# Kernel tuning notes

Hardware: AMD Instinct MI355X
Metric: run time of the kernel (lower is better)

Reference implementation:

```python
import jax, jax.numpy as jnp
import numpy as np

B, N, C = 4, 4096, 768
H = 8
HD = C // H  # head_dim = 96
SCALE = HD ** -0.5
EPS = 1e-12  # torch F.normalize eps


def setup_inputs() -> dict:
    key = jax.random.key(0)
    ks = jax.random.split(key, 6)
    s = C ** -0.5
    return {
        "context_x": jax.random.normal(ks[0], (B, N, C), dtype=jnp.float32),
        "depth_x": jax.random.normal(ks[1], (B, N, C), dtype=jnp.float32),
        "Wq": jax.random.normal(ks[2], (C, C), dtype=jnp.float32) * s,
        "Wkv": jax.random.normal(ks[3], (C, 2 * C), dtype=jnp.float32) * s,
        "Wproj": jax.random.normal(ks[4], (C, C), dtype=jnp.float32) * s,
        "bproj": jax.random.normal(ks[5], (C,), dtype=jnp.float32) * 0.01,
    }


def _l2norm(x):
    # matches torch.nn.functional.normalize(x, dim=-1)
    n = jnp.sqrt(jnp.sum(x * x, axis=-1, keepdims=True))
    return x / jnp.maximum(n, EPS)


def reference(context_x, depth_x, Wq, Wkv, Wproj, bproj):
    b, n, c = context_x.shape
    # projections
    q = (context_x @ Wq).reshape(b, n, H, HD).transpose(0, 2, 3, 1)  # [B,H,hd,N]
    kv = (depth_x @ Wkv).reshape(b, n, 2, H, HD)
    k = kv[:, :, 0].transpose(0, 2, 3, 1)  # [B,H,hd,N]
    v = kv[:, :, 1].transpose(0, 2, 3, 1)  # [B,H,hd,N]
    # cosine-normalize over the token axis (last dim after transpose)
    q = _l2norm(q)
    k = _l2norm(k)
    # channel-attention (cross-covariance): attn is [B,H,hd,hd]
    attn = jnp.einsum("bhdn,bhen->bhde", q, k) * SCALE
    attn = jax.nn.softmax(attn, axis=-1)
    x = jnp.einsum("bhde,bhen->bhdn", attn, v)  # [B,H,hd,N]
    x = x.transpose(0, 3, 1, 2).reshape(b, n, c)  # [B,N,C]
    return x @ Wproj + bproj
```

## Files before the change

kernel.cpp:

```cpp
#include <hip/hip_runtime.h>


using bf16x8 = __attribute__((ext_vector_type(8))) short;
using f32x4  = __attribute__((ext_vector_type(4))) float;

#define SCALE_ 0.10206207261596575f

__device__ __forceinline__ unsigned short f2bf(float f) {
    unsigned int u = __builtin_bit_cast(unsigned int, f);
    u += 0x7FFFu + ((u >> 16) & 1u);
    return (unsigned short)(u >> 16);
}
__device__ __forceinline__ float bf2f(unsigned short h) {
    unsigned int u = ((unsigned int)h) << 16;
    return __builtin_bit_cast(float, u);
}

__device__ __forceinline__ void glds16(const unsigned short* g, unsigned short* l) {
    __builtin_amdgcn_global_load_lds(
        (const __attribute__((address_space(1))) void*)g,
        (__attribute__((address_space(3))) void*)l, 16, 0, 0);
}

__device__ __forceinline__ float ssq8(bf16x8 v) {
    uint4 u = __builtin_bit_cast(uint4, v);
    unsigned a[4] = {u.x, u.y, u.z, u.w};
    float s = 0.f;
    #pragma unroll
    for (int i = 0; i < 4; i++) {
        float lo = __builtin_bit_cast(float, a[i] << 16);
        float hi = __builtin_bit_cast(float, a[i] & 0xFFFF0000u);
        s += lo * lo + hi * hi;
    }
    return s;
}

__global__ void f32_to_bf16_k(const float* __restrict__ in,
                              unsigned short* __restrict__ out)
{
    size_t idx = ((size_t)blockIdx.x * 256 + threadIdx.x) * 8;
    float4 v0 = *(const float4*)&in[idx];
    float4 v1 = *(const float4*)&in[idx + 4];
    unsigned short h[8];
    h[0] = f2bf(v0.x); h[1] = f2bf(v0.y); h[2] = f2bf(v0.z); h[3] = f2bf(v0.w);
    h[4] = f2bf(v1.x); h[5] = f2bf(v1.y); h[6] = f2bf(v1.z); h[7] = f2bf(v1.w);
    *(bf16x8*)&out[idx] = *(bf16x8*)h;
}

__global__ void transpose_to_bf16(const float* __restrict__ W,
                                  unsigned short* __restrict__ Wt,
                                  int K, int N)
{
    __shared__ float tile[32][33];
    int n0 = blockIdx.x * 32, k0 = blockIdx.y * 32;
    int tx = threadIdx.x, ty = threadIdx.y;
    #pragma unroll
    for (int i = 0; i < 32; i += 8)
        tile[ty + i][tx] = W[(size_t)(k0 + ty + i) * N + n0 + tx];
    __syncthreads();
    #pragma unroll
    for (int i = 0; i < 32; i += 8)
        Wt[(size_t)(n0 + ty + i) * K + k0 + tx] = f2bf(tile[tx][ty + i]);
}

template<int MODE>
__global__ __launch_bounds__(256) void gemm_bt(
    const unsigned short* __restrict__ A, const unsigned short* __restrict__ Bt,
    const float* __restrict__ bias, void* __restrict__ out0, void* __restrict__ out1,
    int M, int N, int K)
{
    __shared__ unsigned short As[128 * 32];
    __shared__ unsigned short Bs[128 * 32];

    const int Nt = gridDim.x, Mt = gridDim.y;
    const int lin = blockIdx.y * Nt + blockIdx.x;
    const int xcd = lin & 7, li = lin >> 3;
    const int band = Mt >> 3;
    const int mt = xcd * band + (li % band);
    const int nt = li / band;
    const int bm = mt * 128, bn = nt * 128;

    const int t = threadIdx.x, lane = t & 63, w = t >> 6;
    const int wm = (w >> 1) * 64, wn = (w & 1) * 64;
    const int mf = lane & 15, quad = lane >> 4;

    const int srow = lane & 15, skc = (lane >> 4) * 8;
    const unsigned short* gA = A  + (size_t)(bm + w * 32 + srow) * K + skc;
    const unsigned short* gB = Bt + (size_t)(bn + w * 32 + srow) * K + skc;

    f32x4 acc[4][4] = {};

    for (int k0 = 0; k0 < K; k0 += 32) {
        #pragma unroll
        for (int c = 0; c < 2; c++) {
            glds16(gA + (size_t)(c * 16) * K + k0, &As[(w * 2 + c) * 512]);
            glds16(gB + (size_t)(c * 16) * K + k0, &Bs[(w * 2 + c) * 512]);
        }
        __syncthreads();
        bf16x8 a[4], b[4];
        #pragma unroll
        for (int i = 0; i < 4; i++)
            a[i] = *(const bf16x8*)&As[(((w >> 1) * 4) + i) * 512 + lane * 8];
        #pragma unroll
        for (int j = 0; j < 4; j++)
            b[j] = *(const bf16x8*)&Bs[(((w & 1) * 4) + j) * 512 + lane * 8];
        #pragma unroll
        for (int i = 0; i < 4; i++)
            #pragma unroll
            for (int j = 0; j < 4; j++)
                acc[i][j] = __builtin_amdgcn_mfma_f32_16x16x32_bf16(a[i], b[j], acc[i][j], 0, 0, 0);
        __syncthreads();
    }

    if constexpr (MODE == 2) {
        float* C = (float*)out0;
        #pragma unroll
        for (int i = 0; i < 4; i++) {
            int row0 = bm + wm + i * 16 + quad * 4;
            #pragma unroll
            for (int j = 0; j < 4; j++) {
                int col = bn + wn + j * 16 + mf;
                float bv = bias[col];
                #pragma unroll
                for (int r = 0; r < 4; r++)
                    C[(size_t)(row0 + r) * N + col] = acc[i][j][r] + bv;
            }
        }
    } else {
        unsigned short* Tr = (unsigned short*)out0;
        unsigned short* Vb = (unsigned short*)out1;
        const bool kpart = (MODE == 0) || (bn < 768);
        #pragma unroll
        for (int i = 0; i < 4; i++) {
            int row0 = bm + wm + i * 16 + quad * 4;
            int bb = row0 >> 12, n = row0 & 4095;
            #pragma unroll
            for (int j = 0; j < 4; j++) {
                int c = bn + wn + j * 16 + mf;
                if (kpart) {
                    int h = (c * 683) >> 16;
                    int d = c - h * 96;
                    size_t o = ((size_t)((bb * 8 + h) * 96 + d)) * 4096 + n;
                    ushort4 v4;
                    v4.x = f2bf(acc[i][j][0]); v4.y = f2bf(acc[i][j][1]);
                    v4.z = f2bf(acc[i][j][2]); v4.w = f2bf(acc[i][j][3]);
                    *(ushort4*)&Tr[o] = v4;
                } else {
                    int cv = c - 768;
                    #pragma unroll
                    for (int r = 0; r < 4; r++)
                        Vb[(size_t)(row0 + r) * 768 + cv] = f2bf(acc[i][j][r]);
                }
            }
        }
    }
}

__global__ __launch_bounds__(256) void s_gemm(
    const unsigned short* __restrict__ Qt, const unsigned short* __restrict__ Kt,
    float* __restrict__ Spart, float* __restrict__ ssq)
{
    __shared__ unsigned short Qs[2][12 * 512];
    __shared__ unsigned short Ks[2][12 * 512];
    const int s = blockIdx.x, bh = blockIdx.y;
    const int t = threadIdx.x, lane = t & 63, w = t >> 6;
    const int m0 = (w >> 1) * 48, n0w = (w & 1) * 48;
    const int mf = lane & 15, quad = lane >> 4;
    const int srow = lane & 15, skc = (lane >> 4) * 8;
    const int nwin = s * 512;

    const unsigned short* Qg = Qt + (size_t)bh * 96 * 4096;
    const unsigned short* Kg = Kt + (size_t)bh * 96 * 4096;

    f32x4 acc[3][3] = {};
    float sq[3] = {0.f, 0.f, 0.f}, sk[3] = {0.f, 0.f, 0.f};

    #pragma unroll
    for (int c = 0; c < 3; c++) {
        int bi = w * 3 + c, kc = bi / 6, g = bi % 6;
        size_t go = (size_t)(g * 16 + srow) * 4096 + nwin + kc * 32 + skc;
        glds16(Qg + go, &Qs[0][bi * 512]);
        glds16(Kg + go, &Ks[0][bi * 512]);
    }

    for (int it = 0; it < 8; it++) {
        const int cur = it & 1;
        __syncthreads();
        if (it + 1 < 8) {
            const int nxt = cur ^ 1;
            const int nn = nwin + (it + 1) * 64;
            #pragma unroll
            for (int c = 0; c < 3; c++) {
                int bi = w * 3 + c, kc = bi / 6, g = bi % 6;
                size_t go = (size_t)(g * 16 + srow) * 4096 + nn + kc * 32 + skc;
                glds16(Qg + go, &Qs[nxt][bi * 512]);
                glds16(Kg + go, &Ks[nxt][bi * 512]);
            }
        }
        #pragma unroll
        for (int kk = 0; kk < 2; kk++) {
            bf16x8 a[3], b[3];
            #pragma unroll
            for (int i = 0; i < 3; i++)
                a[i] = *(const bf16x8*)&Qs[cur][(kk * 6 + (w >> 1) * 3 + i) * 512 + lane * 8];
            #pragma unroll
            for (int j = 0; j < 3; j++)
                b[j] = *(const bf16x8*)&Ks[cur][(kk * 6 + (w & 1) * 3 + j) * 512 + lane * 8];
            if ((w & 1) == 0) {
                #pragma unroll
                for (int i = 0; i < 3; i++) sq[i] += ssq8(a[i]);
            }
            if ((w >> 1) == 0) {
                #pragma unroll
                for (int j = 0; j < 3; j++) sk[j] += ssq8(b[j]);
            }
            #pragma unroll
            for (int i = 0; i < 3; i++)
                #pragma unroll
                for (int j = 0; j < 3; j++)
                    acc[i][j] = __builtin_amdgcn_mfma_f32_16x16x32_bf16(a[i], b[j], acc[i][j], 0, 0, 0);
        }
    }

    if ((w & 1) == 0) {
        #pragma unroll
        for (int i = 0; i < 3; i++) {
            float v = sq[i];
            v += __shfl_xor(v, 16, 64);
            v += __shfl_xor(v, 32, 64);
            if (lane < 16) atomicAdd(&ssq[bh * 96 + m0 + i * 16 + lane], v);
        }
    }
    if ((w >> 1) == 0) {
        #pragma unroll
        for (int j = 0; j < 3; j++) {
            float v = sk[j];
            v += __shfl_xor(v, 16, 64);
            v += __shfl_xor(v, 32, 64);
            if (lane < 16) atomicAdd(&ssq[3072 + bh * 96 + n0w + j * 16 + lane], v);
        }
    }

    float* outp = Spart + (size_t)(bh * 8 + s) * 9216;
    #pragma unroll
    for (int i = 0; i < 3; i++)
        #pragma unroll
        for (int j = 0; j < 3; j++) {
            int e  = n0w + j * 16 + mf;
            int d0 = m0 + i * 16 + quad * 4;
            #pragma unroll
            for (int r = 0; r < 4; r++)
                outp[(d0 + r) * 96 + e] = acc[i][j][r];
        }
}

__global__ __launch_bounds__(256) void softmax_k(
    const float* __restrict__ Spart, const float* __restrict__ ssq,
    unsigned short* __restrict__ P)
{
    const int bh = blockIdx.y;
    const int d  = blockIdx.x * 4 + (threadIdx.x >> 6);
    const int lane = threadIdx.x & 63;

    const float sr = SCALE_ / fmaxf(sqrtf(ssq[bh * 96 + d]), 1e-12f);

    const float* Sp = Spart + (size_t)bh * 8 * 9216 + d * 96;
    float sa = 0.f, sb = 0.f;
    #pragma unroll
    for (int ch = 0; ch < 8; ch++) {
        sa += Sp[ch * 9216 + lane];
        if (lane < 32) sb += Sp[ch * 9216 + 64 + lane];
    }
    float ka = 1.0f / fmaxf(sqrtf(ssq[3072 + bh * 96 + lane]), 1e-12f);
    float va = sa * sr * ka;
    float vb = -1e30f;
    if (lane < 32) {
        float kb = 1.0f / fmaxf(sqrtf(ssq[3072 + bh * 96 + 64 + lane]), 1e-12f);
        vb = sb * sr * kb;
    }

    float m = fmaxf(va, vb);
    #pragma unroll
    for (int off = 32; off >= 1; off >>= 1)
        m = fmaxf(m, __shfl_xor(m, off, 64));

    float ea = __expf(va - m);
    float eb = (lane < 32) ? __expf(vb - m) : 0.f;
    float ssum = ea + eb;
    #pragma unroll
    for (int off = 32; off >= 1; off >>= 1)
        ssum += __shfl_xor(ssum, off, 64);

    float inv = 1.0f / ssum;
    unsigned short* Pr = P + (size_t)bh * 9216 + d * 96;
    Pr[lane] = f2bf(ea * inv);
    if (lane < 32) Pr[64 + lane] = f2bf(eb * inv);
}

__global__ __launch_bounds__(256) void pv_gemm(
    const unsigned short* __restrict__ Vb, const unsigned short* __restrict__ P,
    unsigned short* __restrict__ X)
{
    __shared__ unsigned short Ps[96][104];
    int ntile = blockIdx.x, bh = blockIdx.y;
    int b = bh >> 3, h = bh & 7;
    int t = threadIdx.x, lane = t & 63, w = t >> 6;

    const unsigned short* Pg = P + (size_t)bh * 9216;
    #pragma unroll
    for (int i = 0; i < 9; i++) {
        int idx4 = t + 256 * i;
        int row = idx4 / 24, c4 = (idx4 - row * 24) * 4;
        *(ushort4*)&Ps[row][c4] = *(const ushort4*)&Pg[row * 96 + c4];
    }
    __syncthreads();

    const unsigned short* Vbase = Vb + (size_t)b * 4096 * 768 + h * 96;
    int mf = lane & 15, k8 = (lane >> 4) * 8;
    f32x4 acc[2][6] = {};
    #pragma unroll
    for (int k = 0; k < 3; k++) {
        bf16x8 a[2], bb[6];
        #pragma unroll
        for (int i = 0; i < 2; i++) {
            int row = ntile * 128 + w * 32 + i * 16 + mf;
            a[i] = *(const bf16x8*)&Vbase[(size_t)row * 768 + k * 32 + k8];
        }
        #pragma unroll
        for (int j = 0; j < 6; j++)
            bb[j] = *(const bf16x8*)&Ps[j * 16 + mf][k * 32 + k8];
        #pragma unroll
        for (int i = 0; i < 2; i++)
            #pragma unroll
            for (int j = 0; j < 6; j++)
                acc[i][j] = __builtin_amdgcn_mfma_f32_16x16x32_bf16(a[i], bb[j], acc[i][j], 0, 0, 0);
    }
    #pragma unroll
    for (int i = 0; i < 2; i++)
        #pragma unroll
        for (int j = 0; j < 6; j++)
            #pragma unroll
            for (int r = 0; r < 4; r++) {
                int n_tok = ntile * 128 + w * 32 + i * 16 + (lane >> 4) * 4 + r;
                int c = h * 96 + j * 16 + mf;
                X[((size_t)b * 4096 + n_tok) * 768 + c] = f2bf(acc[i][j][r]);
            }
}

extern "C" void kernel_launch(void* const* d_in, const int* in_sizes, int n_in,
                              void* d_out, int out_size, void* d_ws, size_t ws_size,
                              hipStream_t stream)
{
    (void)in_sizes; (void)n_in; (void)out_size; (void)ws_size;
    const float* ctx   = (const float*)d_in[0];
    const float* dep   = (const float*)d_in[1];
    const float* Wq    = (const float*)d_in[2];
    const float* Wkv   = (const float*)d_in[3];
    const float* Wproj = (const float*)d_in[4];
    const float* bproj = (const float*)d_in[5];
    float* out = (float*)d_out;

    char* p = (char*)d_ws;
    auto carve = [&](size_t bytes) {
        char* r = p;
        p += (bytes + 255) & ~(size_t)255;
        return r;
    };
    unsigned short* WqT    = (unsigned short*)carve((size_t)768 * 768 * 2);
    unsigned short* WkvT   = (unsigned short*)carve((size_t)1536 * 768 * 2);
    unsigned short* WprojT = (unsigned short*)carve((size_t)768 * 768 * 2);
    unsigned short* Qt     = (unsigned short*)carve((size_t)32 * 96 * 4096 * 2);
    unsigned short* Kt     = (unsigned short*)carve((size_t)32 * 96 * 4096 * 2);
    unsigned short* Vb     = (unsigned short*)carve((size_t)16384 * 768 * 2);
    unsigned short* Xb     = (unsigned short*)carve((size_t)16384 * 768 * 2);
    float*          ssq    = (float*)carve((size_t)2 * 3072 * 4);
    float*          Spart  = (float*)carve((size_t)32 * 8 * 9216 * 4);
    unsigned short* Pb     = (unsigned short*)carve((size_t)32 * 9216 * 2);
    unsigned short* depB   = (unsigned short*)carve((size_t)16384 * 768 * 2);
    unsigned short* ctxB   = Xb;

    hipMemsetAsync(ssq, 0, 2 * 3072 * 4, stream);

    f32_to_bf16_k<<<6144, 256, 0, stream>>>(ctx, ctxB);
    f32_to_bf16_k<<<6144, 256, 0, stream>>>(dep, depB);

    dim3 tb(32, 8);
    transpose_to_bf16<<<dim3(24, 24), tb, 0, stream>>>(Wq, WqT, 768, 768);
    transpose_to_bf16<<<dim3(48, 24), tb, 0, stream>>>(Wkv, WkvT, 768, 1536);
    transpose_to_bf16<<<dim3(24, 24), tb, 0, stream>>>(Wproj, WprojT, 768, 768);

    gemm_bt<0><<<dim3(6, 128), 256, 0, stream>>>(ctxB, WqT, nullptr, Qt, nullptr, 16384, 768, 768);
    gemm_bt<1><<<dim3(12, 128), 256, 0, stream>>>(depB, WkvT, nullptr, Kt, Vb, 16384, 1536, 768);

    s_gemm<<<dim3(8, 32), 256, 0, stream>>>(Qt, Kt, Spart, ssq);
    softmax_k<<<dim3(24, 32), 256, 0, stream>>>(Spart, ssq, Pb);
    pv_gemm<<<dim3(32, 32), 256, 0, stream>>>(Vb, Pb, Xb);
    gemm_bt<2><<<dim3(6, 128), 256, 0, stream>>>(Xb, WprojT, bproj, out, nullptr, 16384, 768, 768);
}
```

Measured before the change: 237.3 us.

## Rewrite projection GEMMs as 256x256 tiles with double-buffered ping-pong pipeline

Replaces the 128x128, 256-thread, single-buffer GEMM with a 256x256 tile, 512-thread kernel. It double-buffers LDS, splits each 64-wide K step into four MFMA quadrants interleaved with async global-to-LDS loads, and adds explicit vmcnt waits, barriers and setprio to overlap memory with compute. The larger tile raises operand reuse, and the schedule hides load latency. In exchange it uses more LDS and registers (launch bounds 512,2) and gives fewer blocks: 192 or 384 on a 256-CU part, which may hurt occupancy and wave balance.

```diff
diff --git a/kernel.cpp b/kernel.cpp
--- a/kernel.cpp
+++ b/kernel.cpp
@@ -63,14 +63,80 @@
         Wt[(size_t)(n0 + ty + i) * K + k0 + tx] = f2bf(tile[tx][ty + i]);
 }
 
+
+#define BAR __builtin_amdgcn_s_barrier()
+#define VM(n) asm volatile("s_waitcnt vmcnt(" #n ")" ::: "memory")
+
+#define ST_A(buf, tt, h) do { \
+    _Pragma("unroll") \
+    for (int c_ = 0; c_ < 2; c_++) \
+        glds16(gA + (size_t)(((h) * 8 + w) * 16) * K + (size_t)(tt) * 64 + c_ * 32, \
+               &As[buf][(c_ * 16 + (h) * 8 + w) * 512]); \
+} while (0)
+
+#define ST_B(buf, tt, h) do { \
+    _Pragma("unroll") \
+    for (int c_ = 0; c_ < 2; c_++) \
+        glds16(gB + (size_t)(((h) * 8 + w) * 16) * K + (size_t)(tt) * 64 + c_ * 32, \
+               &Bs[buf][(c_ * 16 + (h) * 8 + w) * 512]); \
+} while (0)
+
+#define RD_A(buf, mh) do { \
+    _Pragma("unroll") \
+    for (int i_ = 0; i_ < 4; i_++) \
+    _Pragma("unroll") \
+    for (int kk_ = 0; kk_ < 2; kk_++) \
+        a[i_][kk_] = *(const bf16x8*)&As[buf][(kk_ * 16 + wr * 8 + (mh) * 4 + i_) * 512 + lane * 8]; \
+} while (0)
+
+#define RD_B(buf, nh) do { \
+    _Pragma("unroll") \
+    for (int j_ = 0; j_ < 2; j_++) \
+    _Pragma("unroll") \
+    for (int kk_ = 0; kk_ < 2; kk_++) \
+        b[nh][j_][kk_] = *(const bf16x8*)&Bs[buf][(kk_ * 16 + wc * 4 + (nh) * 2 + j_) * 512 + lane * 8]; \
+} while (0)
+
+#define MM(mh, nh) do { \
+    __builtin_amdgcn_s_setprio(1); \
+    _Pragma("unroll") \
+    for (int i_ = 0; i_ < 4; i_++) \
+    _Pragma("unroll") \
+    for (int j_ = 0; j_ < 2; j_++) \
+    _Pragma("unroll") \
+    for (int kk_ = 0; kk_ < 2; kk_++) \
+        acc[(mh) * 4 + i_][(nh) * 2 + j_] = __builtin_amdgcn_mfma_f32_16x16x32_bf16( \
+            a[i_][kk_], b[nh][j_][kk_], acc[(mh) * 4 + i_][(nh) * 2 + j_], 0, 0, 0); \
+    __builtin_amdgcn_s_setprio(0); \
+} while (0)
+
+#define KITER(t0v, LAST) do { \
+     RD_A(0, 0); RD_B(0, 0); ST_B(1, (t0v) + 1, 0); \
+             BAR; MM(0, 0); BAR; \
+     RD_B(0, 1); ST_B(1, (t0v) + 1, 1); \
+             BAR; MM(0, 1); VM(6); BAR; \
+     RD_A(0, 1); ST_A(1, (t0v) + 1, 1); \
+             BAR; MM(1, 0); BAR; \
+     if (!(LAST)) ST_A(0, (t0v) + 2, 0); \
+             BAR; MM(1, 1); if (LAST) { VM(2); } else { VM(4); } BAR; \
+     RD_A(1, 0); RD_B(1, 0); if (!(LAST)) ST_B(0, (t0v) + 2, 0); \
+             BAR; MM(0, 0); BAR; \
+     RD_B(1, 1); if (!(LAST)) ST_B(0, (t0v) + 2, 1); \
+             BAR; MM(0, 1); if (LAST) { VM(0); } else { VM(6); } BAR; \
+     RD_A(1, 1); if (!(LAST)) ST_A(0, (t0v) + 2, 1); \
+             BAR; MM(1, 0); BAR; \
+     if (!(LAST)) { ST_A(1, (t0v) + 3, 0); } \
+             BAR; MM(1, 1); if (!(LAST)) { VM(4); } BAR; \
+} while (0)
+
 template<int MODE>
-__global__ __launch_bounds__(256) void gemm_bt(
+__global__ __launch_bounds__(512, 2) void gemm_bt(
     const unsigned short* __restrict__ A, const unsigned short* __restrict__ Bt,
     const float* __restrict__ bias, void* __restrict__ out0, void* __restrict__ out1,
     int M, int N, int K)
 {
-    __shared__ unsigned short As[128 * 32];
-    __shared__ unsigned short Bs[128 * 32];
+    __shared__ unsigned short As[2][32 * 512];
+    __shared__ unsigned short Bs[2][32 * 512];
 
     const int Nt = gridDim.x, Mt = gridDim.y;
     const int lin = blockIdx.y * Nt + blockIdx.x;
@@ -78,48 +144,35 @@
     const int band = Mt >> 3;
     const int mt = xcd * band + (li % band);
     const int nt = li / band;
-    const int bm = mt * 128, bn = nt * 128;
+    const int bm = mt * 256, bn = nt * 256;
 
     const int t = threadIdx.x, lane = t & 63, w = t >> 6;
-    const int wm = (w >> 1) * 64, wn = (w & 1) * 64;
+    const int wr = w >> 2, wc = w & 3;
     const int mf = lane & 15, quad = lane >> 4;
-
     const int srow = lane & 15, skc = (lane >> 4) * 8;
-    const unsigned short* gA = A  + (size_t)(bm + w * 32 + srow) * K + skc;
-    const unsigned short* gB = Bt + (size_t)(bn + w * 32 + srow) * K + skc;
-
-    f32x4 acc[4][4] = {};
-
-    for (int k0 = 0; k0 < K; k0 += 32) {
-        #pragma unroll
-        for (int c = 0; c < 2; c++) {
-            glds16(gA + (size_t)(c * 16) * K + k0, &As[(w * 2 + c) * 512]);
-            glds16(gB + (size_t)(c * 16) * K + k0, &Bs[(w * 2 + c) * 512]);
-        }
-        __syncthreads();
-        bf16x8 a[4], b[4];
-        #pragma unroll
-        for (int i = 0; i < 4; i++)
-            a[i] = *(const bf16x8*)&As[(((w >> 1) * 4) + i) * 512 + lane * 8];
-        #pragma unroll
-        for (int j = 0; j < 4; j++)
-            b[j] = *(const bf16x8*)&Bs[(((w & 1) * 4) + j) * 512 + lane * 8];
-        #pragma unroll
-        for (int i = 0; i < 4; i++)
-            #pragma unroll
-            for (int j = 0; j < 4; j++)
-                acc[i][j] = __builtin_amdgcn_mfma_f32_16x16x32_bf16(a[i], b[j], acc[i][j], 0, 0, 0);
-        __syncthreads();
-    }
+
+    const unsigned short* gA = A  + (size_t)(bm + srow) * K + skc;
+    const unsigned short* gB = Bt + (size_t)(bn + srow) * K + skc;
+
+    f32x4 acc[8][4] = {};
+    bf16x8 a[4][2], b[2][2][2];
+
+    const int NIT = K >> 7;
+
+    ST_A(0, 0, 0); ST_A(0, 0, 1); ST_B(0, 0, 0); ST_B(0, 0, 1); ST_A(1, 1, 0);
+    VM(2); BAR;
+
+    for (int it = 0; it < NIT - 1; ++it) { KITER(2 * it, false); }
+    KITER(2 * (NIT - 1), true);
 
     if constexpr (MODE == 2) {
         float* C = (float*)out0;
         #pragma unroll
-        for (int i = 0; i < 4; i++) {
-            int row0 = bm + wm + i * 16 + quad * 4;
+        for (int i = 0; i < 8; i++) {
+            int row0 = bm + wr * 128 + i * 16 + quad * 4;
             #pragma unroll
             for (int j = 0; j < 4; j++) {
-                int col = bn + wn + j * 16 + mf;
+                int col = bn + wc * 64 + j * 16 + mf;
                 float bv = bias[col];
                 #pragma unroll
                 for (int r = 0; r < 4; r++)
@@ -131,12 +184,12 @@
         unsigned short* Vb = (unsigned short*)out1;
         const bool kpart = (MODE == 0) || (bn < 768);
         #pragma unroll
-        for (int i = 0; i < 4; i++) {
-            int row0 = bm + wm + i * 16 + quad * 4;
+        for (int i = 0; i < 8; i++) {
+            int row0 = bm + wr * 128 + i * 16 + quad * 4;
             int bb = row0 >> 12, n = row0 & 4095;
             #pragma unroll
             for (int j = 0; j < 4; j++) {
-                int c = bn + wn + j * 16 + mf;
+                int c = bn + wc * 64 + j * 16 + mf;
                 if (kpart) {
                     int h = (c * 683) >> 16;
                     int d = c - h * 96;
@@ -155,6 +208,15 @@
         }
     }
 }
+
+#undef KITER
+#undef MM
+#undef RD_A
+#undef RD_B
+#undef ST_A
+#undef ST_B
+#undef VM
+#undef BAR
 
 __global__ __launch_bounds__(256) void s_gemm(
     const unsigned short* __restrict__ Qt, const unsigned short* __restrict__ Kt,
@@ -389,11 +451,11 @@
     transpose_to_bf16<<<dim3(48, 24), tb, 0, stream>>>(Wkv, WkvT, 768, 1536);
     transpose_to_bf16<<<dim3(24, 24), tb, 0, stream>>>(Wproj, WprojT, 768, 768);
 
-    gemm_bt<0><<<dim3(6, 128), 256, 0, stream>>>(ctxB, WqT, nullptr, Qt, nullptr, 16384, 768, 768);
-    gemm_bt<1><<<dim3(12, 128), 256, 0, stream>>>(depB, WkvT, nullptr, Kt, Vb, 16384, 1536, 768);
+    gemm_bt<0><<<dim3(3, 64), 512, 0, stream>>>(ctxB, WqT, nullptr, Qt, nullptr, 16384, 768, 768);
+    gemm_bt<1><<<dim3(6, 64), 512, 0, stream>>>(depB, WkvT, nullptr, Kt, Vb, 16384, 1536, 768);
 
     s_gemm<<<dim3(8, 32), 256, 0, stream>>>(Qt, Kt, Spart, ssq);
     softmax_k<<<dim3(24, 32), 256, 0, stream>>>(Spart, ssq, Pb);
     pv_gemm<<<dim3(32, 32), 256, 0, stream>>>(Vb, Pb, Xb);
-    gemm_bt<2><<<dim3(6, 128), 256, 0, stream>>>(Xb, WprojT, bproj, out, nullptr, 16384, 768, 768);
-}
+    gemm_bt<2><<<dim3(3, 64), 512, 0, stream>>>(Xb, WprojT, bproj, out, nullptr, 16384, 768, 768);
+}
```

Result: slower. 245.8 us (+3.6%).

## Triple-buffer projection GEMM LDS loads with prefetch depth two

Applied to the files above, without the earlier changes.

Rewrites the projection GEMM main loop to use three LDS buffers with async global-to-LDS loads issued two K-steps ahead. Each step waits with explicit vmcnt counts and a single barrier, replacing the two syncthreads per step. The change also raises MFMA issue priority around the compute block and hardcodes K=768. Loads should then overlap with matrix math, at the cost of three times the LDS per block and a kernel that only handles K=768.

```diff
diff --git a/kernel.cpp b/kernel.cpp
--- a/kernel.cpp
+++ b/kernel.cpp
@@ -5,6 +5,7 @@
 using f32x4  = __attribute__((ext_vector_type(4))) float;
 
 #define SCALE_ 0.10206207261596575f
+#define KD 768
 
 __device__ __forceinline__ unsigned short f2bf(float f) {
     unsigned int u = __builtin_bit_cast(unsigned int, f);
@@ -63,14 +64,26 @@
         Wt[(size_t)(n0 + ty + i) * K + k0 + tx] = f2bf(tile[tx][ty + i]);
 }
 
+
+#define BAR __builtin_amdgcn_s_barrier()
+#define VM(n) asm volatile("s_waitcnt vmcnt(" #n ")" ::: "memory")
+
+#define ST(tt, bi) do { \
+    _Pragma("unroll") \
+    for (int c_ = 0; c_ < 2; c_++) { \
+        glds16(gA + (size_t)(c_ * 16) * KD + (tt) * 32, &As[bi][(w * 2 + c_) * 512]); \
+        glds16(gB + (size_t)(c_ * 16) * KD + (tt) * 32, &Bs[bi][(w * 2 + c_) * 512]); \
+    } \
+} while (0)
+
 template<int MODE>
-__global__ __launch_bounds__(256) void gemm_bt(
+__global__ __launch_bounds__(256, 3) void gemm_bt(
     const unsigned short* __restrict__ A, const unsigned short* __restrict__ Bt,
     const float* __restrict__ bias, void* __restrict__ out0, void* __restrict__ out1,
-    int M, int N, int K)
-{
-    __shared__ unsigned short As[128 * 32];
-    __shared__ unsigned short Bs[128 * 32];
+    int M, int N)
+{
+    __shared__ unsigned short As[3][4096];
+    __shared__ unsigned short Bs[3][4096];
 
     const int Nt = gridDim.x, Mt = gridDim.y;
     const int lin = blockIdx.y * Nt + blockIdx.x;
@@ -81,45 +94,54 @@
     const int bm = mt * 128, bn = nt * 128;
 
     const int t = threadIdx.x, lane = t & 63, w = t >> 6;
-    const int wm = (w >> 1) * 64, wn = (w & 1) * 64;
     const int mf = lane & 15, quad = lane >> 4;
-
     const int srow = lane & 15, skc = (lane >> 4) * 8;
-    const unsigned short* gA = A  + (size_t)(bm + w * 32 + srow) * K + skc;
-    const unsigned short* gB = Bt + (size_t)(bn + w * 32 + srow) * K + skc;
+
+    const unsigned short* gA = A  + (size_t)(bm + w * 32 + srow) * KD + skc;
+    const unsigned short* gB = Bt + (size_t)(bn + w * 32 + srow) * KD + skc;
 
     f32x4 acc[4][4] = {};
 
-    for (int k0 = 0; k0 < K; k0 += 32) {
-        #pragma unroll
-        for (int c = 0; c < 2; c++) {
-            glds16(gA + (size_t)(c * 16) * K + k0, &As[(w * 2 + c) * 512]);
-            glds16(gB + (size_t)(c * 16) * K + k0, &Bs[(w * 2 + c) * 512]);
-        }
-        __syncthreads();
+    ST(0, 0); ST(1, 1);
+    VM(4);
+    BAR;
+
+    int cur = 0;
+    #pragma unroll 1
+    for (int tt = 0; tt < 24; ++tt) {
+        int nb = cur - 1; if (nb < 0) nb = 2;
+        if (tt < 22) ST(tt + 2, nb);
+
         bf16x8 a[4], b[4];
         #pragma unroll
         for (int i = 0; i < 4; i++)
-            a[i] = *(const bf16x8*)&As[(((w >> 1) * 4) + i) * 512 + lane * 8];
+            a[i] = *(const bf16x8*)&As[cur][(((w >> 1) * 4) + i) * 512 + lane * 8];
         #pragma unroll
         for (int j = 0; j < 4; j++)
-            b[j] = *(const bf16x8*)&Bs[(((w & 1) * 4) + j) * 512 + lane * 8];
+            b[j] = *(const bf16x8*)&Bs[cur][(((w & 1) * 4) + j) * 512 + lane * 8];
+
+        __builtin_amdgcn_s_setprio(1);
         #pragma unroll
         for (int i = 0; i < 4; i++)
             #pragma unroll
             for (int j = 0; j < 4; j++)
                 acc[i][j] = __builtin_amdgcn_mfma_f32_16x16x32_bf16(a[i], b[j], acc[i][j], 0, 0, 0);
-        __syncthreads();
+        __builtin_amdgcn_s_setprio(0);
+
+        if (tt < 22) { VM(4); }
+        else if (tt == 22) { VM(0); }
+        BAR;
+        cur = cur + 1; if (cur == 3) cur = 0;
     }
 
     if constexpr (MODE == 2) {
         float* C = (float*)out0;
         #pragma unroll
         for (int i = 0; i < 4; i++) {
-            int row0 = bm + wm + i * 16 + quad * 4;
+            int row0 = bm + (w >> 1) * 64 + i * 16 + quad * 4;
             #pragma unroll
             for (int j = 0; j < 4; j++) {
-                int col = bn + wn + j * 16 + mf;
+                int col = bn + (w & 1) * 64 + j * 16 + mf;
                 float bv = bias[col];
                 #pragma unroll
                 for (int r = 0; r < 4; r++)
@@ -132,11 +154,11 @@
         const bool kpart = (MODE == 0) || (bn < 768);
         #pragma unroll
         for (int i = 0; i < 4; i++) {
-            int row0 = bm + wm + i * 16 + quad * 4;
+            int row0 = bm + (w >> 1) * 64 + i * 16 + quad * 4;
             int bb = row0 >> 12, n = row0 & 4095;
             #pragma unroll
             for (int j = 0; j < 4; j++) {
-                int c = bn + wn + j * 16 + mf;
+                int c = bn + (w & 1) * 64 + j * 16 + mf;
                 if (kpart) {
                     int h = (c * 683) >> 16;
                     int d = c - h * 96;
@@ -155,6 +177,10 @@
         }
     }
 }
+
+#undef ST
+#undef VM
+#undef BAR
 
 __global__ __launch_bounds__(256) void s_gemm(
     const unsigned short* __restrict__ Qt, const unsigned short* __restrict__ Kt,
@@ -389,11 +415,11 @@
     transpose_to_bf16<<<dim3(48, 24), tb, 0, stream>>>(Wkv, WkvT, 768, 1536);
     transpose_to_bf16<<<dim3(24, 24), tb, 0, stream>>>(Wproj, WprojT, 768, 768);
 
-    gemm_bt<0><<<dim3(6, 128), 256, 0, stream>>>(ctxB, WqT, nullptr, Qt, nullptr, 16384, 768, 768);
-    gemm_bt<1><<<dim3(12, 128), 256, 0, stream>>>(depB, WkvT, nullptr, Kt, Vb, 16384, 1536, 768);
+    gemm_bt<0><<<dim3(6, 128), 256, 0, stream>>>(ctxB, WqT, nullptr, Qt, nullptr, 16384, 768);
+    gemm_bt<1><<<dim3(12, 128), 256, 0, stream>>>(depB, WkvT, nullptr, Kt, Vb, 16384, 1536);
 
     s_gemm<<<dim3(8, 32), 256, 0, stream>>>(Qt, Kt, Spart, ssq);
     softmax_k<<<dim3(24, 32), 256, 0, stream>>>(Spart, ssq, Pb);
     pv_gemm<<<dim3(32, 32), 256, 0, stream>>>(Vb, Pb, Xb);
-    gemm_bt<2><<<dim3(6, 128), 256, 0, stream>>>(Xb, WprojT, bproj, out, nullptr, 16384, 768, 768);
-}
+    gemm_bt<2><<<dim3(6, 128), 256, 0, stream>>>(Xb, WprojT, bproj, out, nullptr, 16384, 768);
+}
```

Result: no change. 238.7 us (+0.6%).
